# Performance work log

Hardware: AMD Instinct MI355X
Metric: run time of the kernel (lower is better)

## Reference

```python
import jax, jax.numpy as jnp
import numpy as np

HIDDEN = 2048
NUM_HEADS = 16
HEAD_DIM = HIDDEN // NUM_HEADS
INTER = 8192
EPS = 1e-6


def setup_inputs() -> dict:
    key = jax.random.key(0)
    ks = jax.random.split(key, 10)
    s = 0.02
    return {
        "x": jax.random.normal(ks[0], (2, 2048, HIDDEN), dtype=jnp.float32),
        "w_ln1": jnp.ones((HIDDEN,), dtype=jnp.float32),
        "wq": jax.random.normal(ks[1], (HIDDEN, HIDDEN), dtype=jnp.float32) * s,
        "wk": jax.random.normal(ks[2], (HIDDEN, HIDDEN), dtype=jnp.float32) * s,
        "wv": jax.random.normal(ks[3], (HIDDEN, HIDDEN), dtype=jnp.float32) * s,
        "wo": jax.random.normal(ks[4], (HIDDEN, HIDDEN), dtype=jnp.float32) * s,
        "w_ln2": jnp.ones((HIDDEN,), dtype=jnp.float32),
        "wg": jax.random.normal(ks[5], (INTER, HIDDEN), dtype=jnp.float32) * s,
        "wu": jax.random.normal(ks[6], (INTER, HIDDEN), dtype=jnp.float32) * s,
        "wd": jax.random.normal(ks[7], (HIDDEN, INTER), dtype=jnp.float32) * s,
    }


def rmsnorm(x, w):
    rms = jnp.sqrt(jnp.mean(x * x, axis=-1, keepdims=True) + EPS)
    return x / rms * w


def attention(x, wq, wk, wv, wo):
    B, T, C = x.shape
    # weights are [out, in] (torch Linear convention) -> x @ W.T
    q = (x @ wq.T).reshape(B, T, NUM_HEADS, HEAD_DIM)
    k = (x @ wk.T).reshape(B, T, NUM_HEADS, HEAD_DIM)
    v = (x @ wv.T).reshape(B, T, NUM_HEADS, HEAD_DIM)
    scores = jnp.einsum("bqhd,bkhd->bhqk", q, k) / jnp.sqrt(jnp.float32(HEAD_DIM))
    attn = jax.nn.softmax(scores, axis=-1)
    out = jnp.einsum("bhqk,bkhd->bqhd", attn, v).reshape(B, T, C)
    return out @ wo.T


def mlp(x, wg, wu, wd):
    return (jax.nn.silu(x @ wg.T) * (x @ wu.T)) @ wd.T


def reference(x, w_ln1, wq, wk, wv, wo, w_ln2, wg, wu, wd):
    x = x + attention(rmsnorm(x, w_ln1), wq, wk, wv, wo)
    x = x + mlp(rmsnorm(x, w_ln2), wg, wu, wd)
    return x
```

## Files before the change

### kernel.cpp

```cpp
#include <hip/hip_runtime.h>
#include <stdint.h>

typedef unsigned short u16;
typedef unsigned int   u32;
typedef short s16x8 __attribute__((ext_vector_type(8)));
typedef u16   u16x8 __attribute__((ext_vector_type(8)));
typedef float f32x4 __attribute__((ext_vector_type(4)));

__device__ __forceinline__ u16 f2bf(float f) {
    u32 u = __float_as_uint(f);
    u32 r = u + 0x7fffu + ((u >> 16) & 1u);
    return (u16)(r >> 16);
}
__device__ __forceinline__ float bf2f(u16 h) {
    return __uint_as_float(((u32)h) << 16);
}

#define GLD16(gp, lp) __builtin_amdgcn_global_load_lds(                          \
    (const __attribute__((address_space(1))) void*)(uintptr_t)(gp),             \
    (__attribute__((address_space(3))) void*)(u32)(uintptr_t)(lp), 16, 0, 0)

#define FENCE asm volatile("" ::: "memory")

template<int N> __device__ __forceinline__ void waitv() {
    if constexpr (N == 0)      asm volatile("s_waitcnt vmcnt(0)" ::: "memory");
    else if constexpr (N == 3) asm volatile("s_waitcnt vmcnt(3)" ::: "memory");
    else                       asm volatile("s_waitcnt vmcnt(4)" ::: "memory");
}

__global__ __launch_bounds__(256)
void cast_w(const float* __restrict__ in, u16* __restrict__ out, int n)
{
    const int i = (blockIdx.x * 256 + threadIdx.x) * 8;
    if (i >= n) return;
    f32x4 a = *(const f32x4*)(in + i);
    f32x4 b = *(const f32x4*)(in + i + 4);
    u16x8 o;
    o[0] = f2bf(a[0]); o[1] = f2bf(a[1]); o[2] = f2bf(a[2]); o[3] = f2bf(a[3]);
    o[4] = f2bf(b[0]); o[5] = f2bf(b[1]); o[6] = f2bf(b[2]); o[7] = f2bf(b[3]);
    *(u16x8*)(out + i) = o;
}

__global__ __launch_bounds__(256)
void rmsnorm_k(const float* __restrict__ x, const float* __restrict__ wln,
               u16* __restrict__ out, int C)
{
    const int row = blockIdx.x;
    const int tid = threadIdx.x;
    const float* xr = x + (size_t)row * C;
    f32x4 a = *(const f32x4*)(xr + tid * 8);
    f32x4 b = *(const f32x4*)(xr + tid * 8 + 4);
    float s = a[0]*a[0] + a[1]*a[1] + a[2]*a[2] + a[3]*a[3]
            + b[0]*b[0] + b[1]*b[1] + b[2]*b[2] + b[3]*b[3];
    #pragma unroll
    for (int off = 1; off < 64; off <<= 1) s += __shfl_xor(s, off);
    __shared__ float red[4];
    if ((tid & 63) == 0) red[tid >> 6] = s;
    __syncthreads();
    float tot = red[0] + red[1] + red[2] + red[3];
    float inv = rsqrtf(tot / (float)C + 1e-6f);
    f32x4 wa = *(const f32x4*)(wln + tid * 8);
    f32x4 wb = *(const f32x4*)(wln + tid * 8 + 4);
    u16x8 o;
    o[0] = f2bf(a[0]*inv*wa[0]); o[1] = f2bf(a[1]*inv*wa[1]);
    o[2] = f2bf(a[2]*inv*wa[2]); o[3] = f2bf(a[3]*inv*wa[3]);
    o[4] = f2bf(b[0]*inv*wb[0]); o[5] = f2bf(b[1]*inv*wb[1]);
    o[6] = f2bf(b[2]*inv*wb[2]); o[7] = f2bf(b[3]*inv*wb[3]);
    *(u16x8*)(out + (size_t)row * C + tid * 8) = o;
}

template<int MODE, int MR>
__global__ __launch_bounds__(512, 1)
void gemm8(const u16* __restrict__ A, const u16* __restrict__ W,
           const float* __restrict__ resid, const u16* __restrict__ aux,
           void* __restrict__ Cout, int M, int N, int K, float scale)
{
    constexpr int BM  = MR * 32;
    constexpr int MR2 = MR / 2;
    constexpr int SRA = MR * 8;
    constexpr int AL  = BM / 128;
    constexpr int WS  = 2 + AL;
    __shared__ __align__(16) u16 lds[2][(BM + 256) * 64];

    const int tid  = threadIdx.x;
    const int lane = tid & 63;
    const int w    = tid >> 6;
    const int wm   = w >> 2;
    const int wn   = w & 3;

    const int gx  = N >> 8;
    const int nwg = gridDim.x;
    const int sid = ((int)blockIdx.x & 7) * (nwg >> 3) + ((int)blockIdx.x >> 3);
    const int brow = (sid / gx) * BM;
    const int bcol = (sid % gx) * 256;

    const int KT = K >> 6;
    const int NI = KT >> 1;

    f32x4 acc[MR][4] = {};

    auto stageA = [&](int buf, int g, int kt) {
        #pragma unroll
        for (int j = 0; j < AL; ++j) {
            const int p   = j * 64 + (tid >> 3);
            const int row = ((p & ~(SRA - 1)) << 1) | (g * SRA) | (p & (SRA - 1));
            const int ch  = (tid & 7) ^ (row & 7);
            const u16* src = A + (size_t)(brow + row) * K + kt * 64 + ch * 8;
            const int p0  = j * 64 + (w << 3);
            const int r0  = ((p0 & ~(SRA - 1)) << 1) | (g * SRA) | (p0 & (SRA - 1));
            GLD16(src, &lds[buf][0] + r0 * 64);
        }
    };
    auto stageB = [&](int buf, int g, int kt) {
        #pragma unroll
        for (int j = 0; j < 2; ++j) {
            const int p   = j * 64 + (tid >> 3);
            const int row = ((p & ~31) << 1) | (g * 32) | (p & 31);
            const int ch  = (tid & 7) ^ (row & 7);
            const u16* src = W + (size_t)(bcol + row) * K + kt * 64 + ch * 8;
            const int p0  = j * 64 + (w << 3);
            const int r0  = ((p0 & ~31) << 1) | (g * 32) | (p0 & 31);
            GLD16(src, &lds[buf][BM * 64] + r0 * 64);
        }
    };

#define PHASE(BUF, MH, NH, STAGE, ENDWAIT)                                       \
    {                                                                            \
        const u16* Ab = &lds[BUF][0];                                            \
        const u16* Bb = &lds[BUF][BM * 64];                                      \
        s16x8 af[MR2][2], bfr[2][2];                                             \
        _Pragma("unroll") for (int f = 0; f < MR2; ++f)                          \
        _Pragma("unroll") for (int ks = 0; ks < 2; ++ks) {                       \
            const int row = wm * (BM / 2) + (MH) * (BM / 4) + f * 16 + (lane & 15); \
            const int ch  = (ks * 4 + (lane >> 4)) ^ (row & 7);                  \
            af[f][ks] = *(const s16x8*)(Ab + row * 64 + ch * 8);                 \
        }                                                                        \
        _Pragma("unroll") for (int g = 0; g < 2; ++g)                            \
        _Pragma("unroll") for (int ks = 0; ks < 2; ++ks) {                       \
            const int row = wn * 64 + (NH) * 32 + g * 16 + (lane & 15);          \
            const int ch  = (ks * 4 + (lane >> 4)) ^ (row & 7);                  \
            bfr[g][ks] = *(const s16x8*)(Bb + row * 64 + ch * 8);                \
        }                                                                        \
        STAGE;                                                                   \
        ENDWAIT;                                                                 \
        FENCE; __builtin_amdgcn_s_barrier(); FENCE;                              \
        __builtin_amdgcn_s_setprio(1);                                           \
        _Pragma("unroll") for (int f = 0; f < MR2; ++f)                          \
        _Pragma("unroll") for (int g = 0; g < 2; ++g)                            \
        _Pragma("unroll") for (int ks = 0; ks < 2; ++ks)                         \
            acc[(MH) * MR2 + f][(NH) * 2 + g] =                                  \
                __builtin_amdgcn_mfma_f32_16x16x32_bf16(                         \
                    af[f][ks], bfr[g][ks], acc[(MH) * MR2 + f][(NH) * 2 + g],    \
                    0, 0, 0);                                                    \
        __builtin_amdgcn_s_setprio(0);                                           \
        asm volatile("s_waitcnt lgkmcnt(0)" ::: "memory");                       \
        FENCE; __builtin_amdgcn_s_barrier(); FENCE;                              \
    }

    stageB(0, 0, 0); stageA(0, 1, 0); stageA(0, 0, 0); stageB(0, 1, 0);
    stageB(1, 0, 1); stageA(1, 1, 1);
    waitv<WS>();
    FENCE; __builtin_amdgcn_s_barrier(); FENCE;

    for (int it = 0; it < NI; ++it) {
        const int t1  = 2 * it + 1;
        const int t0n = 2 * it + 2;
        const int t1n = 2 * it + 3;
        const bool s0 = t0n < KT, s1 = t1n < KT;
        const bool last = (it == NI - 1);

        PHASE(0, 0, 0, { stageB(1, 1, t1); }, {})
        PHASE(0, 1, 0, { stageA(1, 0, t1); }, {})
        PHASE(0, 1, 1, { if (s0) stageB(0, 0, t0n); }, {})
        PHASE(0, 0, 1, { if (s0) stageA(0, 1, t0n); },
              { if (last) waitv<0>(); else waitv<WS>(); })
        PHASE(1, 0, 0, { if (s0) stageA(0, 0, t0n); }, {})
        PHASE(1, 1, 0, { if (s0) stageB(0, 1, t0n); }, {})
        PHASE(1, 1, 1, { if (s1) stageB(1, 0, t1n); }, {})
        PHASE(1, 0, 1, { if (s1) stageA(1, 1, t1n); },
              { if (!last) waitv<WS>(); })
    }
#undef PHASE

    const int er = (lane >> 4) * 4;
    const int ec = lane & 15;
    #pragma unroll
    for (int i = 0; i < MR; ++i) {
        #pragma unroll
        for (int j = 0; j < 4; ++j) {
            #pragma unroll
            for (int r = 0; r < 4; ++r) {
                const int row = brow + wm * (BM / 2) + i * 16 + er + r;
                const int col = bcol + wn * 64 + j * 16 + ec;
                const size_t idx = (size_t)row * N + col;
                const float va = acc[i][j][r];
                if (MODE == 0)      ((u16*)Cout)[idx] = f2bf(va);
                else if (MODE == 1) ((u16*)Cout)[idx] = f2bf(va * scale);
                else if (MODE == 2) ((float*)Cout)[idx] = resid[idx] + va;
                else {
                    const float g  = bf2f(aux[idx]);
                    const float sg = g / (1.0f + exp2f(-g * 1.4426950408889634f));
                    ((u16*)Cout)[idx] = f2bf(sg * va);
                }
            }
        }
    }
}

__global__ __launch_bounds__(256)
void flash_attn(const u16* __restrict__ q, const u16* __restrict__ k,
                const u16* __restrict__ vT, u16* __restrict__ o)
{
    __shared__ __align__(16) u16 Kt[64 * 128];
    __shared__ __align__(16) u16 Vt[128 * 64];
    __shared__ __align__(16) u16 Pw[4][16 * 64];
    const int tid  = threadIdx.x;
    const int lane = tid & 63;
    const int w    = tid >> 6;
    const int qtile = blockIdx.x;
    const int bh    = blockIdx.y;
    const int b = bh >> 4, h = bh & 15;
    const size_t head  = ((size_t)b * 2048) * 2048 + (size_t)h * 128;
    const size_t vbase = ((size_t)h * 128) * 4096 + (size_t)b * 2048;

    const int tq = qtile * 64 + w * 16 + (lane & 15);
    const u16* qp = q + head + (size_t)tq * 2048 + (lane >> 4) * 8;
    s16x8 qf[4];
    #pragma unroll
    for (int dk = 0; dk < 4; ++dk) qf[dk] = *(const s16x8*)(qp + dk * 32);

    f32x4 oa[8] = {};
    float m_r[4] = {-1e30f, -1e30f, -1e30f, -1e30f};
    float l_r[4] = {0.f, 0.f, 0.f, 0.f};

    const int ksr = tid >> 4;
    const int ksc = (tid & 15) * 8;
    const int vd  = tid >> 1;
    const int vk0 = (tid & 1) * 32;

    char* KtB = (char*)Kt;
    char* VtB = (char*)Vt;
    char* PwB = (char*)&Pw[w][0];

    const u16* vrow = vT + vbase + (size_t)vd * 4096 + vk0;

    for (int kb = 0; kb < 32; ++kb) {
        const int k0 = kb * 64;
        __syncthreads();
        #pragma unroll
        for (int rr = 0; rr < 4; ++rr) {
            const int row = rr * 16 + ksr;
            s16x8 t = *(const s16x8*)(k + head + (size_t)(k0 + row) * 2048 + ksc);
            *(s16x8*)(KtB + ((row * 256 + ksc * 2) ^ ((row & 7) << 4))) = t;
        }
        #pragma unroll
        for (int c = 0; c < 4; ++c) {
            s16x8 t = *(const s16x8*)(vrow + k0 + c * 8);
            *(s16x8*)(VtB + ((vd * 128 + vk0 * 2 + c * 16) ^ ((vd & 7) << 4))) = t;
        }
        __syncthreads();

        f32x4 s[4] = {};
        __builtin_amdgcn_s_setprio(1);
        #pragma unroll
        for (int kt = 0; kt < 4; ++kt) {
            const int row = kt * 16 + (lane & 15);
            #pragma unroll
            for (int dk = 0; dk < 4; ++dk) {
                const int dcol = dk * 32 + (lane >> 4) * 8;
                s16x8 kf = *(const s16x8*)(KtB + ((row * 256 + dcol * 2) ^ ((row & 7) << 4)));
                s[kt] = __builtin_amdgcn_mfma_f32_16x16x32_bf16(qf[dk], kf, s[kt], 0, 0, 0);
            }
        }
        __builtin_amdgcn_s_setprio(0);

        float mx[4];
        #pragma unroll
        for (int r = 0; r < 4; ++r) {
            float m0 = fmaxf(fmaxf(s[0][r], s[1][r]), fmaxf(s[2][r], s[3][r]));
            m0 = fmaxf(m0, __shfl_xor(m0, 1));
            m0 = fmaxf(m0, __shfl_xor(m0, 2));
            m0 = fmaxf(m0, __shfl_xor(m0, 4));
            m0 = fmaxf(m0, __shfl_xor(m0, 8));
            mx[r] = m0;
        }
        const bool grow = (mx[0] > m_r[0] + 8.f) || (mx[1] > m_r[1] + 8.f) ||
                          (mx[2] > m_r[2] + 8.f) || (mx[3] > m_r[3] + 8.f);
        if (__any(grow)) {
            #pragma unroll
            for (int r = 0; r < 4; ++r) {
                const float mn = fmaxf(m_r[r], mx[r]);
                const float sc = exp2f(m_r[r] - mn);
                m_r[r] = mn;
                l_r[r] *= sc;
                #pragma unroll
                for (int ni = 0; ni < 8; ++ni) oa[ni][r] *= sc;
            }
        }
        #pragma unroll
        for (int r = 0; r < 4; ++r) {
            const float p0 = exp2f(s[0][r] - m_r[r]);
            const float p1 = exp2f(s[1][r] - m_r[r]);
            const float p2 = exp2f(s[2][r] - m_r[r]);
            const float p3 = exp2f(s[3][r] - m_r[r]);
            s[0][r] = p0; s[1][r] = p1; s[2][r] = p2; s[3][r] = p3;
            float sum = p0 + p1 + p2 + p3;
            sum += __shfl_xor(sum, 1);
            sum += __shfl_xor(sum, 2);
            sum += __shfl_xor(sum, 4);
            sum += __shfl_xor(sum, 8);
            l_r[r] += sum;
        }
        #pragma unroll
        for (int kt = 0; kt < 4; ++kt) {
            const int kc = kt * 16 + (lane & 15);
            #pragma unroll
            for (int r = 0; r < 4; ++r) {
                const int qr = (lane >> 4) * 4 + r;
                *(u16*)(PwB + ((qr * 128 + kc * 2) ^ (((qr >> 2) & 3) << 5))) = f2bf(s[kt][r]);
            }
        }
        __builtin_amdgcn_s_setprio(1);
        #pragma unroll
        for (int kt2 = 0; kt2 < 2; ++kt2) {
            const int qrow = lane & 15;
            const int keyb = kt2 * 32 + (lane >> 4) * 8;
            s16x8 pf = *(const s16x8*)(PwB + ((qrow * 128 + keyb * 2) ^ (((qrow >> 2) & 3) << 5)));
            #pragma unroll
            for (int ni = 0; ni < 8; ++ni) {
                const int dd = ni * 16 + (lane & 15);
                s16x8 vf = *(const s16x8*)(VtB + ((dd * 128 + keyb * 2) ^ ((dd & 7) << 4)));
                oa[ni] = __builtin_amdgcn_mfma_f32_16x16x32_bf16(pf, vf, oa[ni], 0, 0, 0);
            }
        }
        __builtin_amdgcn_s_setprio(0);
    }
    #pragma unroll
    for (int r = 0; r < 4; ++r) {
        const float inv = 1.0f / l_r[r];
        const int tout = qtile * 64 + w * 16 + (lane >> 4) * 4 + r;
        u16* op = o + head + (size_t)tout * 2048 + (lane & 15);
        #pragma unroll
        for (int ni = 0; ni < 8; ++ni)
            op[ni * 16] = f2bf(oa[ni][r] * inv);
    }
}

extern "C" void kernel_launch(void* const* d_in, const int* in_sizes, int n_in,
                              void* d_out, int out_size, void* d_ws, size_t ws_size,
                              hipStream_t stream)
{
    (void)in_sizes; (void)n_in; (void)out_size; (void)ws_size;
    const float* x    = (const float*)d_in[0];
    const float* wln1 = (const float*)d_in[1];
    const float* wq   = (const float*)d_in[2];
    const float* wk   = (const float*)d_in[3];
    const float* wv   = (const float*)d_in[4];
    const float* wo   = (const float*)d_in[5];
    const float* wln2 = (const float*)d_in[6];
    const float* wg   = (const float*)d_in[7];
    const float* wu   = (const float*)d_in[8];
    const float* wd   = (const float*)d_in[9];
    float* out = (float*)d_out;

    const size_t MB = 1024ull * 1024ull;
    char* ws = (char*)d_ws;
    u16*   arena = (u16*)(ws + 0);
    float* hbuf  = (float*)(ws + 32 * MB);
    u16*   xn    = (u16*)(ws + 64 * MB);
    u16*   qb    = (u16*)(ws + 80 * MB);
    u16*   kbuf  = (u16*)(ws + 96 * MB);
    u16*   vT    = (u16*)(ws + 112 * MB);
    u16*   abuf  = (u16*)(ws + 128 * MB);
    u16*   gbuf  = (u16*)(ws + 80 * MB);

    const int M = 4096, C = 2048, I = 8192;
    const float qscale = 0.1275164899f;
    dim3 blk(256);
    dim3 blk8(512);

    rmsnorm_k<<<M, blk, 0, stream>>>(x, wln1, xn, C);

    cast_w<<<(C * C) / 2048, blk, 0, stream>>>(wq, arena, C * C);
    gemm8<1, 4><<<dim3((C / 256) * (M / 128)), blk8, 0, stream>>>(xn, arena, nullptr, nullptr, qb, M, C, C, qscale);
    cast_w<<<(C * C) / 2048, blk, 0, stream>>>(wk, arena, C * C);
    gemm8<0, 4><<<dim3((C / 256) * (M / 128)), blk8, 0, stream>>>(xn, arena, nullptr, nullptr, kbuf, M, C, C, 1.f);
    cast_w<<<(C * C) / 2048, blk, 0, stream>>>(wv, arena, C * C);
    gemm8<0, 4><<<dim3((M / 256) * (C / 128)), blk8, 0, stream>>>(arena, xn, nullptr, nullptr, vT, C, M, C, 1.f);

    flash_attn<<<dim3(2048 / 64, 32), blk, 0, stream>>>(qb, kbuf, vT, abuf);

    cast_w<<<(C * C) / 2048, blk, 0, stream>>>(wo, arena, C * C);
    gemm8<2, 4><<<dim3((C / 256) * (M / 128)), blk8, 0, stream>>>(abuf, arena, x, nullptr, hbuf, M, C, C, 1.f);

    rmsnorm_k<<<M, blk, 0, stream>>>(hbuf, wln2, xn, C);

    cast_w<<<(I * C) / 2048, blk, 0, stream>>>(wg, arena, I * C);
    gemm8<0, 8><<<dim3((I / 256) * (M / 256)), blk8, 0, stream>>>(xn, arena, nullptr, nullptr, gbuf, M, I, C, 1.f);
    cast_w<<<(I * C) / 2048, blk, 0, stream>>>(wu, arena, I * C);
    gemm8<3, 8><<<dim3((I / 256) * (M / 256)), blk8, 0, stream>>>(xn, arena, nullptr, gbuf, gbuf, M, I, C, 1.f);
    cast_w<<<(C * I) / 2048, blk, 0, stream>>>(wd, arena, C * I);
    gemm8<2, 4><<<dim3((C / 256) * (M / 128)), blk8, 0, stream>>>(gbuf, arena, hbuf, nullptr, out, M, C, I, 1.f);
}
```

Baseline: 871.3 us.

## Enlarge flash attention tile to 256 queries with double-buffered K/V prefetch

The flash attention kernel now uses 512 threads per block, and each wave handles 32 query rows instead of 16, so each K/V tile loaded into LDS feeds twice as many MFMAs. K and V are double-buffered in LDS, and the next tile is prefetched into registers while the current one is computed, which leaves one barrier per iteration. The aim is to cut global and LDS traffic for K/V and to hide load latency. In exchange the grid is smaller (256 blocks) with launch_bounds(512,1), and register pressure per wave is higher, which could lower occupancy or cause spills.

```diff
diff --git a/kernel.cpp b/kernel.cpp
--- a/kernel.cpp
+++ b/kernel.cpp
@@ -207,13 +207,13 @@
     }
 }
 
-__global__ __launch_bounds__(256)
+__global__ __launch_bounds__(512, 1)
 void flash_attn(const u16* __restrict__ q, const u16* __restrict__ k,
                 const u16* __restrict__ vT, u16* __restrict__ o)
 {
-    __shared__ __align__(16) u16 Kt[64 * 128];
-    __shared__ __align__(16) u16 Vt[128 * 64];
-    __shared__ __align__(16) u16 Pw[4][16 * 64];
+    __shared__ __align__(16) u16 Kt[2][64 * 128];
+    __shared__ __align__(16) u16 Vt[2][128 * 64];
+    __shared__ __align__(16) u16 Pw[8][32 * 64];
     const int tid  = threadIdx.x;
     const int lane = tid & 63;
     const int w    = tid >> 6;
@@ -223,126 +223,156 @@
     const size_t head  = ((size_t)b * 2048) * 2048 + (size_t)h * 128;
     const size_t vbase = ((size_t)h * 128) * 4096 + (size_t)b * 2048;
 
-    const int tq = qtile * 64 + w * 16 + (lane & 15);
-    const u16* qp = q + head + (size_t)tq * 2048 + (lane >> 4) * 8;
-    s16x8 qf[4];
+    s16x8 qf[2][4];
     #pragma unroll
-    for (int dk = 0; dk < 4; ++dk) qf[dk] = *(const s16x8*)(qp + dk * 32);
-
-    f32x4 oa[8] = {};
-    float m_r[4] = {-1e30f, -1e30f, -1e30f, -1e30f};
-    float l_r[4] = {0.f, 0.f, 0.f, 0.f};
-
-    const int ksr = tid >> 4;
-    const int ksc = (tid & 15) * 8;
-    const int vd  = tid >> 1;
-    const int vk0 = (tid & 1) * 32;
-
-    char* KtB = (char*)Kt;
-    char* VtB = (char*)Vt;
+    for (int qi = 0; qi < 2; ++qi) {
+        const int tq = qtile * 256 + w * 32 + qi * 16 + (lane & 15);
+        const u16* qp = q + head + (size_t)tq * 2048 + (lane >> 4) * 8;
+        #pragma unroll
+        for (int dk = 0; dk < 4; ++dk) qf[qi][dk] = *(const s16x8*)(qp + dk * 32);
+    }
+
+    f32x4 oa[2][8] = {};
+    float m_r[2][4] = {{-1e30f,-1e30f,-1e30f,-1e30f},{-1e30f,-1e30f,-1e30f,-1e30f}};
+    float l_r[2][4] = {};
+
+    const int krow = tid >> 3;
+    const int kcol = (tid & 7) * 16;
+    const int vd   = tid >> 2;
+    const int vk   = (tid & 3) * 16;
+    const u16* kg = k + head + (size_t)krow * 2048 + kcol;
+    const u16* vg = vT + vbase + (size_t)vd * 4096 + vk;
+    const u32 kw0 = (u32)((krow * 256 + kcol * 2)      ^ ((krow & 7) << 4));
+    const u32 kw1 = (u32)((krow * 256 + kcol * 2 + 16) ^ ((krow & 7) << 4));
+    const u32 vw0 = (u32)((vd * 128 + vk * 2)          ^ ((vd & 7) << 4));
+    const u32 vw1 = (u32)((vd * 128 + vk * 2 + 16)     ^ ((vd & 7) << 4));
+
     char* PwB = (char*)&Pw[w][0];
 
-    const u16* vrow = vT + vbase + (size_t)vd * 4096 + vk0;
+    s16x8 kr0 = *(const s16x8*)(kg);
+    s16x8 kr1 = *(const s16x8*)(kg + 8);
+    s16x8 vr0 = *(const s16x8*)(vg);
+    s16x8 vr1 = *(const s16x8*)(vg + 8);
 
     for (int kb = 0; kb < 32; ++kb) {
-        const int k0 = kb * 64;
-        __syncthreads();
-        #pragma unroll
-        for (int rr = 0; rr < 4; ++rr) {
-            const int row = rr * 16 + ksr;
-            s16x8 t = *(const s16x8*)(k + head + (size_t)(k0 + row) * 2048 + ksc);
-            *(s16x8*)(KtB + ((row * 256 + ksc * 2) ^ ((row & 7) << 4))) = t;
-        }
-        #pragma unroll
-        for (int c = 0; c < 4; ++c) {
-            s16x8 t = *(const s16x8*)(vrow + k0 + c * 8);
-            *(s16x8*)(VtB + ((vd * 128 + vk0 * 2 + c * 16) ^ ((vd & 7) << 4))) = t;
-        }
-        __syncthreads();
-
-        f32x4 s[4] = {};
+        const int cur = kb & 1;
+        char* KtB = (char*)&Kt[cur][0];
+        char* VtB = (char*)&Vt[cur][0];
+        *(s16x8*)(KtB + kw0) = kr0;
+        *(s16x8*)(KtB + kw1) = kr1;
+        *(s16x8*)(VtB + vw0) = vr0;
+        *(s16x8*)(VtB + vw1) = vr1;
+        if (kb + 1 < 32) {
+            const int k0n = (kb + 1) * 64;
+            kr0 = *(const s16x8*)(kg + (size_t)k0n * 2048);
+            kr1 = *(const s16x8*)(kg + (size_t)k0n * 2048 + 8);
+            vr0 = *(const s16x8*)(vg + k0n);
+            vr1 = *(const s16x8*)(vg + k0n + 8);
+        }
+        asm volatile("s_waitcnt lgkmcnt(0)" ::: "memory");
+        __builtin_amdgcn_s_barrier();
+        FENCE;
+
+        f32x4 s[2][4] = {};
         __builtin_amdgcn_s_setprio(1);
         #pragma unroll
         for (int kt = 0; kt < 4; ++kt) {
             const int row = kt * 16 + (lane & 15);
+            s16x8 kf[4];
             #pragma unroll
             for (int dk = 0; dk < 4; ++dk) {
                 const int dcol = dk * 32 + (lane >> 4) * 8;
-                s16x8 kf = *(const s16x8*)(KtB + ((row * 256 + dcol * 2) ^ ((row & 7) << 4)));
-                s[kt] = __builtin_amdgcn_mfma_f32_16x16x32_bf16(qf[dk], kf, s[kt], 0, 0, 0);
-            }
+                kf[dk] = *(const s16x8*)(KtB + ((row * 256 + dcol * 2) ^ ((row & 7) << 4)));
+            }
+            #pragma unroll
+            for (int qi = 0; qi < 2; ++qi)
+                #pragma unroll
+                for (int dk = 0; dk < 4; ++dk)
+                    s[qi][kt] = __builtin_amdgcn_mfma_f32_16x16x32_bf16(qf[qi][dk], kf[dk], s[qi][kt], 0, 0, 0);
         }
         __builtin_amdgcn_s_setprio(0);
 
-        float mx[4];
-        #pragma unroll
-        for (int r = 0; r < 4; ++r) {
-            float m0 = fmaxf(fmaxf(s[0][r], s[1][r]), fmaxf(s[2][r], s[3][r]));
-            m0 = fmaxf(m0, __shfl_xor(m0, 1));
-            m0 = fmaxf(m0, __shfl_xor(m0, 2));
-            m0 = fmaxf(m0, __shfl_xor(m0, 4));
-            m0 = fmaxf(m0, __shfl_xor(m0, 8));
-            mx[r] = m0;
-        }
-        const bool grow = (mx[0] > m_r[0] + 8.f) || (mx[1] > m_r[1] + 8.f) ||
-                          (mx[2] > m_r[2] + 8.f) || (mx[3] > m_r[3] + 8.f);
-        if (__any(grow)) {
+        #pragma unroll
+        for (int qi = 0; qi < 2; ++qi) {
+            float mx[4];
             #pragma unroll
             for (int r = 0; r < 4; ++r) {
-                const float mn = fmaxf(m_r[r], mx[r]);
-                const float sc = exp2f(m_r[r] - mn);
-                m_r[r] = mn;
-                l_r[r] *= sc;
+                float m0 = fmaxf(fmaxf(s[qi][0][r], s[qi][1][r]), fmaxf(s[qi][2][r], s[qi][3][r]));
+                m0 = fmaxf(m0, __shfl_xor(m0, 1));
+                m0 = fmaxf(m0, __shfl_xor(m0, 2));
+                m0 = fmaxf(m0, __shfl_xor(m0, 4));
+                m0 = fmaxf(m0, __shfl_xor(m0, 8));
+                mx[r] = m0;
+            }
+            const bool grow = (mx[0] > m_r[qi][0] + 8.f) || (mx[1] > m_r[qi][1] + 8.f) ||
+                              (mx[2] > m_r[qi][2] + 8.f) || (mx[3] > m_r[qi][3] + 8.f);
+            if (__any(grow)) {
                 #pragma unroll
-                for (int ni = 0; ni < 8; ++ni) oa[ni][r] *= sc;
-            }
-        }
-        #pragma unroll
-        for (int r = 0; r < 4; ++r) {
-            const float p0 = exp2f(s[0][r] - m_r[r]);
-            const float p1 = exp2f(s[1][r] - m_r[r]);
-            const float p2 = exp2f(s[2][r] - m_r[r]);
-            const float p3 = exp2f(s[3][r] - m_r[r]);
-            s[0][r] = p0; s[1][r] = p1; s[2][r] = p2; s[3][r] = p3;
-            float sum = p0 + p1 + p2 + p3;
-            sum += __shfl_xor(sum, 1);
-            sum += __shfl_xor(sum, 2);
-            sum += __shfl_xor(sum, 4);
-            sum += __shfl_xor(sum, 8);
-            l_r[r] += sum;
-        }
-        #pragma unroll
-        for (int kt = 0; kt < 4; ++kt) {
-            const int kc = kt * 16 + (lane & 15);
+                for (int r = 0; r < 4; ++r) {
+                    const float mn = fmaxf(m_r[qi][r], mx[r]);
+                    const float sc = exp2f(m_r[qi][r] - mn);
+                    m_r[qi][r] = mn;
+                    l_r[qi][r] *= sc;
+                    #pragma unroll
+                    for (int ni = 0; ni < 8; ++ni) oa[qi][ni][r] *= sc;
+                }
+            }
             #pragma unroll
             for (int r = 0; r < 4; ++r) {
-                const int qr = (lane >> 4) * 4 + r;
-                *(u16*)(PwB + ((qr * 128 + kc * 2) ^ (((qr >> 2) & 3) << 5))) = f2bf(s[kt][r]);
+                const float p0 = exp2f(s[qi][0][r] - m_r[qi][r]);
+                const float p1 = exp2f(s[qi][1][r] - m_r[qi][r]);
+                const float p2 = exp2f(s[qi][2][r] - m_r[qi][r]);
+                const float p3 = exp2f(s[qi][3][r] - m_r[qi][r]);
+                s[qi][0][r] = p0; s[qi][1][r] = p1; s[qi][2][r] = p2; s[qi][3][r] = p3;
+                float sum = p0 + p1 + p2 + p3;
+                sum += __shfl_xor(sum, 1);
+                sum += __shfl_xor(sum, 2);
+                sum += __shfl_xor(sum, 4);
+                sum += __shfl_xor(sum, 8);
+                l_r[qi][r] += sum;
+            }
+            #pragma unroll
+            for (int kt = 0; kt < 4; ++kt) {
+                const int kc = kt * 16 + (lane & 15);
+                #pragma unroll
+                for (int r = 0; r < 4; ++r) {
+                    const int qr = qi * 16 + (lane >> 4) * 4 + r;
+                    *(u16*)(PwB + ((qr * 128 + kc * 2) ^ (((qr >> 2) & 3) << 5))) = f2bf(s[qi][kt][r]);
+                }
             }
         }
         __builtin_amdgcn_s_setprio(1);
         #pragma unroll
         for (int kt2 = 0; kt2 < 2; ++kt2) {
-            const int qrow = lane & 15;
             const int keyb = kt2 * 32 + (lane >> 4) * 8;
-            s16x8 pf = *(const s16x8*)(PwB + ((qrow * 128 + keyb * 2) ^ (((qrow >> 2) & 3) << 5)));
+            s16x8 pf[2];
+            #pragma unroll
+            for (int qi = 0; qi < 2; ++qi) {
+                const int qrow = qi * 16 + (lane & 15);
+                pf[qi] = *(const s16x8*)(PwB + ((qrow * 128 + keyb * 2) ^ (((qrow >> 2) & 3) << 5)));
+            }
             #pragma unroll
             for (int ni = 0; ni < 8; ++ni) {
                 const int dd = ni * 16 + (lane & 15);
                 s16x8 vf = *(const s16x8*)(VtB + ((dd * 128 + keyb * 2) ^ ((dd & 7) << 4)));
-                oa[ni] = __builtin_amdgcn_mfma_f32_16x16x32_bf16(pf, vf, oa[ni], 0, 0, 0);
+                #pragma unroll
+                for (int qi = 0; qi < 2; ++qi)
+                    oa[qi][ni] = __builtin_amdgcn_mfma_f32_16x16x32_bf16(pf[qi], vf, oa[qi][ni], 0, 0, 0);
             }
         }
         __builtin_amdgcn_s_setprio(0);
     }
     #pragma unroll
-    for (int r = 0; r < 4; ++r) {
-        const float inv = 1.0f / l_r[r];
-        const int tout = qtile * 64 + w * 16 + (lane >> 4) * 4 + r;
-        u16* op = o + head + (size_t)tout * 2048 + (lane & 15);
-        #pragma unroll
-        for (int ni = 0; ni < 8; ++ni)
-            op[ni * 16] = f2bf(oa[ni][r] * inv);
+    for (int qi = 0; qi < 2; ++qi) {
+        #pragma unroll
+        for (int r = 0; r < 4; ++r) {
+            const float inv = 1.0f / l_r[qi][r];
+            const int tout = qtile * 256 + w * 32 + qi * 16 + (lane >> 4) * 4 + r;
+            u16* op = o + head + (size_t)tout * 2048 + (lane & 15);
+            #pragma unroll
+            for (int ni = 0; ni < 8; ++ni)
+                op[ni * 16] = f2bf(oa[qi][ni][r] * inv);
+        }
     }
 }
 
@@ -388,7 +418,7 @@
     cast_w<<<(C * C) / 2048, blk, 0, stream>>>(wv, arena, C * C);
     gemm8<0, 4><<<dim3((M / 256) * (C / 128)), blk8, 0, stream>>>(arena, xn, nullptr, nullptr, vT, C, M, C, 1.f);
 
-    flash_attn<<<dim3(2048 / 64, 32), blk, 0, stream>>>(qb, kbuf, vT, abuf);
+    flash_attn<<<dim3(2048 / 256, 32), blk8, 0, stream>>>(qb, kbuf, vT, abuf);
 
     cast_w<<<(C * C) / 2048, blk, 0, stream>>>(wo, arena, C * C);
     gemm8<2, 4><<<dim3((C / 256) * (M / 128)), blk8, 0, stream>>>(abuf, arena, x, nullptr, hbuf, M, C, C, 1.f);
```

Measured after the change: 823.0 us. -5.5%, faster.
